# Kernel tuning notes

Hardware: AMD Instinct MI355X
Metric: run time of the kernel (lower is better)

## Reference

```python
import jax, jax.numpy as jnp
import numpy as np

N = 50000   # nodes
E = 800000  # edges
H = 128     # hidden dim
V = 50000   # feats_per_node (embedding vocab)


def setup_inputs() -> dict:
    key = jax.random.key(0)
    ks = jax.random.split(key, 16)
    s = 0.05  # keep activations in a sane range
    return {
        "node_ids": jax.random.randint(ks[0], (N,), 0, V),
        "src": jax.random.randint(ks[1], (E,), 0, N),
        "dst": jnp.sort(jax.random.randint(ks[2], (E,), 0, N)),
        "emb": jax.random.normal(ks[3], (V, H), jnp.float32) * s,
        "W_pool1": jax.random.normal(ks[4], (H, H), jnp.float32) * s,
        "b_pool1": jax.random.normal(ks[5], (H,), jnp.float32) * s,
        "W_self1": jax.random.normal(ks[6], (H, H), jnp.float32) * s,
        "W_neigh1": jax.random.normal(ks[7], (H, H), jnp.float32) * s,
        "b1": jax.random.normal(ks[8], (H,), jnp.float32) * s,
        "W_pool2": jax.random.normal(ks[9], (H, H), jnp.float32) * s,
        "b_pool2": jax.random.normal(ks[10], (H,), jnp.float32) * s,
        "W_self2": jax.random.normal(ks[11], (H, H), jnp.float32) * s,
        "W_neigh2": jax.random.normal(ks[12], (H, H), jnp.float32) * s,
        "b2": jax.random.normal(ks[13], (H,), jnp.float32) * s,
    }


def _sage_pool_layer(h, src, dst, W_pool, b_pool, W_self, W_neigh, b):
    # DGL SAGEConv('pool'): per-src MLP, gather over edges, segmented max per dst.
    m = jax.nn.relu(h @ W_pool + b_pool)              # [N, H]
    msgs = m[src]                                     # [E, H] gather
    agg = jax.ops.segment_max(msgs, dst, num_segments=N,
                              indices_are_sorted=True)  # [N, H]
    agg = jnp.where(jnp.isneginf(agg), 0.0, agg)      # zero-in-degree -> 0 (DGL semantics)
    return h @ W_self + agg @ W_neigh + b


def reference(node_ids, src, dst, emb,
              W_pool1, b_pool1, W_self1, W_neigh1, b1,
              W_pool2, b_pool2, W_self2, W_neigh2, b2):
    h = emb[node_ids]                                 # embedding_h on 1-hot indices
    h = _sage_pool_layer(h, src, dst, W_pool1, b_pool1, W_self1, W_neigh1, b1)
    h = _sage_pool_layer(h, src, dst, W_pool2, b_pool2, W_self2, W_neigh2, b2)
    return h
```

## Files before the change

### kernel.cpp

```cpp
#include <hip/hip_runtime.h>

#define HD 128

typedef __attribute__((ext_vector_type(8))) short short8;
typedef __attribute__((ext_vector_type(4))) float floatx4;

typedef unsigned short ushort_t;
typedef unsigned int uint_t;

__device__ __forceinline__ ushort_t f2b(float f) {
    union { float f; uint_t u; } v; v.f = f;
    uint_t r = v.u + 0x7fff + ((v.u >> 16) & 1);
    return (ushort_t)(r >> 16);
}
__device__ __forceinline__ float b_lo(uint_t p) {
    union { uint_t u; float f; } v; v.u = p << 16; return v.f;
}
__device__ __forceinline__ float b_hi(uint_t p) {
    union { uint_t u; float f; } v; v.u = p & 0xffff0000u; return v.f;
}
__device__ __forceinline__ uint_t packb(float a, float b) {
    union { float f; uint_t u; } x, y; x.f = a; y.f = b;
    return (x.u >> 16) | (y.u & 0xffff0000u);
}
__device__ __forceinline__ short8 cvt8(const float* __restrict__ p) {
    float4 u = *(const float4*)p, v = *(const float4*)(p + 4);
    short8 r;
    r[0] = (short)f2b(u.x); r[1] = (short)f2b(u.y); r[2] = (short)f2b(u.z); r[3] = (short)f2b(u.w);
    r[4] = (short)f2b(v.x); r[5] = (short)f2b(v.y); r[6] = (short)f2b(v.z); r[7] = (short)f2b(v.w);
    return r;
}

__global__ __launch_bounds__(256) void k_prep(const int* __restrict__ dst, int E,
                                              int* __restrict__ rp, int N,
                                              const float* W0, const float* W1,
                                              const float* W2, const float* W3,
                                              const float* W4, const float* W5,
                                              ushort_t* __restrict__ Wpk, int nbR) {
    int b = blockIdx.x;
    if (b < nbR) {
        int i = b * 256 + threadIdx.x;
        if (i > N) return;
        int lo = 0, hi = E;
        while (lo < hi) {
            int mid = (lo + hi) >> 1;
            if (dst[mid] < i) lo = mid + 1; else hi = mid;
        }
        rp[i] = lo;
    } else {
        int bb = b - nbR;
        const float* Ws[6] = {W0, W1, W2, W3, W4, W5};
        int mat = bb >> 6;
        int o = ((bb & 63) << 8) + threadIdx.x;
        int j = o & 7, l = (o >> 3) & 63, s = (o >> 9) & 3, t = o >> 11;
        int k = s * 32 + ((l >> 4) & 3) * 8 + j;
        int n = t * 16 + (l & 15);
        Wpk[(size_t)mat * 16384 + o] = f2b(Ws[mat][k * HD + n]);
    }
}

__device__ __forceinline__ void stage_w(const ushort_t* __restrict__ g,
                                        ushort_t* l, int tid) {
#pragma unroll
    for (int i = 0; i < 8; ++i) {
        int off = i * 2048 + tid * 8;
        *(short8*)&l[off] = *(const short8*)&g[off];
    }
}

__global__ __launch_bounds__(256) void k_gather_pool(const int* __restrict__ ids,
                                                     const float* __restrict__ emb,
                                                     const ushort_t* __restrict__ Wpk,
                                                     const float* __restrict__ bias,
                                                     ushort_t* __restrict__ h0,
                                                     ushort_t* __restrict__ m, int N) {
    __shared__ ushort_t Wl[16384];
    stage_w(Wpk, Wl, threadIdx.x);
    __syncthreads();

    int wave = blockIdx.x * 4 + (threadIdx.x >> 6);
    int row0 = wave * 32;
    if (row0 >= N) return;
    int l = threadIdx.x & 63;
    int ar0 = row0 + (l & 15); if (ar0 >= N) ar0 = N - 1;
    int ar1 = ar0 + 16;        if (ar1 >= N) ar1 = N - 1;
    int ac = (l >> 4) * 8;
    int id0 = ids[ar0], id1 = ids[ar1];
    short8 a0[4], a1[4];
#pragma unroll
    for (int s = 0; s < 4; ++s) {
        a0[s] = cvt8(&emb[(size_t)id0 * HD + s * 32 + ac]);
        a1[s] = cvt8(&emb[(size_t)id1 * HD + s * 32 + ac]);
        *(short8*)&h0[(size_t)ar0 * HD + s * 32 + ac] = a0[s];
        *(short8*)&h0[(size_t)ar1 * HD + s * 32 + ac] = a1[s];
    }
    int rb = row0 + (l >> 4) * 4;
#pragma unroll
    for (int t = 0; t < 8; ++t) {
        floatx4 acc0 = {0.f, 0.f, 0.f, 0.f};
        floatx4 acc1 = {0.f, 0.f, 0.f, 0.f};
#pragma unroll
        for (int s = 0; s < 4; ++s) {
            short8 b = *(const short8*)&Wl[(t * 4 + s) * 512 + l * 8];
            acc0 = __builtin_amdgcn_mfma_f32_16x16x32_bf16(a0[s], b, acc0, 0, 0, 0);
            acc1 = __builtin_amdgcn_mfma_f32_16x16x32_bf16(a1[s], b, acc1, 0, 0, 0);
        }
        int col = t * 16 + (l & 15);
        float bv = bias[col];
#pragma unroll
        for (int r = 0; r < 4; ++r) {
            int g0 = rb + r, g1 = rb + 16 + r;
            if (g0 < N) m[(size_t)g0 * HD + col] = f2b(fmaxf(acc0[r] + bv, 0.f));
            if (g1 < N) m[(size_t)g1 * HD + col] = f2b(fmaxf(acc1[r] + bv, 0.f));
        }
    }
}

__global__ __launch_bounds__(256) void k_pool(const ushort_t* __restrict__ h,
                                              const ushort_t* __restrict__ Wpk,
                                              const float* __restrict__ bias,
                                              ushort_t* __restrict__ m, int N) {
    __shared__ ushort_t Wl[16384];
    stage_w(Wpk, Wl, threadIdx.x);
    __syncthreads();

    int wave = blockIdx.x * 4 + (threadIdx.x >> 6);
    int row0 = wave * 32;
    if (row0 >= N) return;
    int l = threadIdx.x & 63;
    int ar0 = row0 + (l & 15); if (ar0 >= N) ar0 = N - 1;
    int ar1 = ar0 + 16;        if (ar1 >= N) ar1 = N - 1;
    int ac = (l >> 4) * 8;
    short8 a0[4], a1[4];
#pragma unroll
    for (int s = 0; s < 4; ++s) {
        a0[s] = *(const short8*)&h[(size_t)ar0 * HD + s * 32 + ac];
        a1[s] = *(const short8*)&h[(size_t)ar1 * HD + s * 32 + ac];
    }
    int rb = row0 + (l >> 4) * 4;
#pragma unroll
    for (int t = 0; t < 8; ++t) {
        floatx4 acc0 = {0.f, 0.f, 0.f, 0.f};
        floatx4 acc1 = {0.f, 0.f, 0.f, 0.f};
#pragma unroll
        for (int s = 0; s < 4; ++s) {
            short8 b = *(const short8*)&Wl[(t * 4 + s) * 512 + l * 8];
            acc0 = __builtin_amdgcn_mfma_f32_16x16x32_bf16(a0[s], b, acc0, 0, 0, 0);
            acc1 = __builtin_amdgcn_mfma_f32_16x16x32_bf16(a1[s], b, acc1, 0, 0, 0);
        }
        int col = t * 16 + (l & 15);
        float bv = bias[col];
#pragma unroll
        for (int r = 0; r < 4; ++r) {
            int g0 = rb + r, g1 = rb + 16 + r;
            if (g0 < N) m[(size_t)g0 * HD + col] = f2b(fmaxf(acc0[r] + bv, 0.f));
            if (g1 < N) m[(size_t)g1 * HD + col] = f2b(fmaxf(acc1[r] + bv, 0.f));
        }
    }
}

__global__ __launch_bounds__(256) void k_segmax(const ushort_t* __restrict__ m,
                                                const int* __restrict__ src,
                                                const int* __restrict__ rp,
                                                ushort_t* __restrict__ agg, int N) {
    int node = blockIdx.x * 4 + (threadIdx.x >> 6);
    if (node >= N) return;
    int l = threadIdx.x & 63;
    int half = l >> 5;
    int col4 = (l & 31) * 4;
    int beg = rp[node], end = rp[node + 1];
    float a0 = 0.f, a1 = 0.f, a2 = 0.f, a3 = 0.f;
    float c0 = 0.f, c1 = 0.f, c2 = 0.f, c3 = 0.f;
    int e = beg;
    for (; e + 8 <= end; e += 8) {
        int e0 = e + half, e1 = e + 2 + half, e2 = e + 4 + half, e3 = e + 6 + half;
        uint2 p0 = *(const uint2*)&m[(size_t)src[e0] * HD + col4];
        uint2 p1 = *(const uint2*)&m[(size_t)src[e1] * HD + col4];
        uint2 p2 = *(const uint2*)&m[(size_t)src[e2] * HD + col4];
        uint2 p3 = *(const uint2*)&m[(size_t)src[e3] * HD + col4];
        a0 = fmaxf(a0, b_lo(p0.x)); a1 = fmaxf(a1, b_hi(p0.x));
        a2 = fmaxf(a2, b_lo(p0.y)); a3 = fmaxf(a3, b_hi(p0.y));
        c0 = fmaxf(c0, b_lo(p1.x)); c1 = fmaxf(c1, b_hi(p1.x));
        c2 = fmaxf(c2, b_lo(p1.y)); c3 = fmaxf(c3, b_hi(p1.y));
        a0 = fmaxf(a0, b_lo(p2.x)); a1 = fmaxf(a1, b_hi(p2.x));
        a2 = fmaxf(a2, b_lo(p2.y)); a3 = fmaxf(a3, b_hi(p2.y));
        c0 = fmaxf(c0, b_lo(p3.x)); c1 = fmaxf(c1, b_hi(p3.x));
        c2 = fmaxf(c2, b_lo(p3.y)); c3 = fmaxf(c3, b_hi(p3.y));
    }
    for (; e < end; e += 2) {
        int ee = e + half; if (ee >= end) ee = end - 1;
        uint2 p = *(const uint2*)&m[(size_t)src[ee] * HD + col4];
        a0 = fmaxf(a0, b_lo(p.x)); a1 = fmaxf(a1, b_hi(p.x));
        a2 = fmaxf(a2, b_lo(p.y)); a3 = fmaxf(a3, b_hi(p.y));
    }
    a0 = fmaxf(a0, c0); a1 = fmaxf(a1, c1); a2 = fmaxf(a2, c2); a3 = fmaxf(a3, c3);
    a0 = fmaxf(a0, __shfl_xor(a0, 32));
    a1 = fmaxf(a1, __shfl_xor(a1, 32));
    a2 = fmaxf(a2, __shfl_xor(a2, 32));
    a3 = fmaxf(a3, __shfl_xor(a3, 32));
    if (half == 0) {
        uint2 o; o.x = packb(a0, a1); o.y = packb(a2, a3);
        *(uint2*)&agg[(size_t)node * HD + col4] = o;
    }
}

template <bool F32OUT>
__global__ __launch_bounds__(256) void k_dual(const ushort_t* __restrict__ h,
                                              const ushort_t* __restrict__ agg,
                                              const ushort_t* __restrict__ WsPk,
                                              const ushort_t* __restrict__ WnPk,
                                              const float* __restrict__ bias,
                                              void* __restrict__ outp, int N) {
    __shared__ ushort_t Wl[32768];
    stage_w(WsPk, Wl, threadIdx.x);
    stage_w(WnPk, Wl + 16384, threadIdx.x);
    __syncthreads();

    int wave = blockIdx.x * 4 + (threadIdx.x >> 6);
    int row0 = wave * 32;
    if (row0 >= N) return;
    int l = threadIdx.x & 63;
    int ar0 = row0 + (l & 15); if (ar0 >= N) ar0 = N - 1;
    int ar1 = ar0 + 16;        if (ar1 >= N) ar1 = N - 1;
    int ac = (l >> 4) * 8;
    short8 ah0[4], ah1[4], ag0[4], ag1[4];
#pragma unroll
    for (int s = 0; s < 4; ++s) {
        ah0[s] = *(const short8*)&h[(size_t)ar0 * HD + s * 32 + ac];
        ah1[s] = *(const short8*)&h[(size_t)ar1 * HD + s * 32 + ac];
        ag0[s] = *(const short8*)&agg[(size_t)ar0 * HD + s * 32 + ac];
        ag1[s] = *(const short8*)&agg[(size_t)ar1 * HD + s * 32 + ac];
    }
    int rb = row0 + (l >> 4) * 4;
#pragma unroll
    for (int t = 0; t < 8; ++t) {
        floatx4 acc0 = {0.f, 0.f, 0.f, 0.f};
        floatx4 acc1 = {0.f, 0.f, 0.f, 0.f};
#pragma unroll
        for (int s = 0; s < 4; ++s) {
            short8 bs = *(const short8*)&Wl[(t * 4 + s) * 512 + l * 8];
            acc0 = __builtin_amdgcn_mfma_f32_16x16x32_bf16(ah0[s], bs, acc0, 0, 0, 0);
            acc1 = __builtin_amdgcn_mfma_f32_16x16x32_bf16(ah1[s], bs, acc1, 0, 0, 0);
        }
#pragma unroll
        for (int s = 0; s < 4; ++s) {
            short8 bn = *(const short8*)&Wl[16384 + (t * 4 + s) * 512 + l * 8];
            acc0 = __builtin_amdgcn_mfma_f32_16x16x32_bf16(ag0[s], bn, acc0, 0, 0, 0);
            acc1 = __builtin_amdgcn_mfma_f32_16x16x32_bf16(ag1[s], bn, acc1, 0, 0, 0);
        }
        int col = t * 16 + (l & 15);
        float bv = bias[col];
#pragma unroll
        for (int r = 0; r < 4; ++r) {
            int g0 = rb + r, g1 = rb + 16 + r;
            float v0 = acc0[r] + bv, v1 = acc1[r] + bv;
            if (F32OUT) {
                if (g0 < N) ((float*)outp)[(size_t)g0 * HD + col] = v0;
                if (g1 < N) ((float*)outp)[(size_t)g1 * HD + col] = v1;
            } else {
                if (g0 < N) ((ushort_t*)outp)[(size_t)g0 * HD + col] = f2b(v0);
                if (g1 < N) ((ushort_t*)outp)[(size_t)g1 * HD + col] = f2b(v1);
            }
        }
    }
}

extern "C" void kernel_launch(void* const* d_in, const int* in_sizes, int n_in,
                              void* d_out, int out_size, void* d_ws, size_t ws_size,
                              hipStream_t stream) {
    const int*   node_ids = (const int*)d_in[0];
    const int*   src      = (const int*)d_in[1];
    const int*   dst      = (const int*)d_in[2];
    const float* emb      = (const float*)d_in[3];
    const float* Wp1      = (const float*)d_in[4];
    const float* bp1      = (const float*)d_in[5];
    const float* Ws1      = (const float*)d_in[6];
    const float* Wn1      = (const float*)d_in[7];
    const float* b1       = (const float*)d_in[8];
    const float* Wp2      = (const float*)d_in[9];
    const float* bp2      = (const float*)d_in[10];
    const float* Ws2      = (const float*)d_in[11];
    const float* Wn2      = (const float*)d_in[12];
    const float* b2       = (const float*)d_in[13];
    float* out = (float*)d_out;

    const int N = in_sizes[0];
    const int E = in_sizes[1];

    char* ws = (char*)d_ws;
    int* rp = (int*)ws;
    size_t off = (((size_t)(N + 1) * 4) + 255) & ~(size_t)255;
    ushort_t* Wpk  = (ushort_t*)(ws + off);
    ushort_t* h0   = Wpk + 6 * 16384;
    ushort_t* h1   = h0 + (size_t)N * HD;
    ushort_t* bufM = h1 + (size_t)N * HD;
    ushort_t* bufA = bufM + (size_t)N * HD;

    const int nbR = (N + 1 + 255) / 256;
    const int nbP = 6 * 64;
    const int nb_gemm = (N + 127) / 128;
    const int nb_seg  = (N + 3) / 4;

    k_prep<<<nbR + nbP, 256, 0, stream>>>(dst, E, rp, N,
                                          Wp1, Ws1, Wn1, Wp2, Ws2, Wn2, Wpk, nbR);

    const ushort_t* Wp1k = Wpk;
    const ushort_t* Ws1k = Wpk + 16384;
    const ushort_t* Wn1k = Wpk + 2 * 16384;
    const ushort_t* Wp2k = Wpk + 3 * 16384;
    const ushort_t* Ws2k = Wpk + 4 * 16384;
    const ushort_t* Wn2k = Wpk + 5 * 16384;

    k_gather_pool<<<nb_gemm, 256, 0, stream>>>(node_ids, emb, Wp1k, bp1, h0, bufM, N);
    k_segmax<<<nb_seg, 256, 0, stream>>>(bufM, src, rp, bufA, N);
    k_dual<false><<<nb_gemm, 256, 0, stream>>>(h0, bufA, Ws1k, Wn1k, b1, h1, N);
    k_pool<<<nb_gemm, 256, 0, stream>>>(h1, Wp2k, bp2, bufM, N);
    k_segmax<<<nb_seg, 256, 0, stream>>>(bufM, src, rp, bufA, N);
    k_dual<true><<<nb_gemm, 256, 0, stream>>>(h1, bufA, Ws2k, Wn2k, b2, out, N);
}
```

Baseline: 236.7 us.

## Transpose MFMA operands for vectorized row stores; widen segmax gathers to 16B

The GEMM kernels swap the MFMA A/B operands so each lane holds four consecutive output columns of one row. The epilogue can then write packed 8-byte bf16 or 16-byte fp32 vectors with a float4 bias load, replacing scattered 2-byte and 4-byte stores. The segmented-max kernel now gathers 16 bytes per lane, with four edges in flight per wave instead of two. That needs an extra shuffle stage and more registers, and wastes more lanes on low-degree tails.

```diff
diff --git a/kernel.cpp b/kernel.cpp
--- a/kernel.cpp
+++ b/kernel.cpp
@@ -68,6 +68,17 @@
     }
 }
 
+__device__ __forceinline__ void store_bf16(ushort_t* __restrict__ m, int row,
+                                           int colbase, const floatx4& acc,
+                                           const float4& bv, bool relu, int N) {
+    if (row >= N) return;
+    float v0 = acc[0] + bv.x, v1 = acc[1] + bv.y, v2 = acc[2] + bv.z, v3 = acc[3] + bv.w;
+    if (relu) { v0 = fmaxf(v0, 0.f); v1 = fmaxf(v1, 0.f); v2 = fmaxf(v2, 0.f); v3 = fmaxf(v3, 0.f); }
+    uint2 o; o.x = (uint_t)f2b(v0) | ((uint_t)f2b(v1) << 16);
+    o.y = (uint_t)f2b(v2) | ((uint_t)f2b(v3) << 16);
+    *(uint2*)&m[(size_t)row * HD + colbase] = o;
+}
+
 __global__ __launch_bounds__(256) void k_gather_pool(const int* __restrict__ ids,
                                                      const float* __restrict__ emb,
                                                      const ushort_t* __restrict__ Wpk,
@@ -94,25 +105,22 @@
         *(short8*)&h0[(size_t)ar0 * HD + s * 32 + ac] = a0[s];
         *(short8*)&h0[(size_t)ar1 * HD + s * 32 + ac] = a1[s];
     }
-    int rb = row0 + (l >> 4) * 4;
+    int g0 = row0 + (l & 15), g1 = g0 + 16;
+    int cb0 = ((l >> 4) & 3) * 4;
 #pragma unroll
     for (int t = 0; t < 8; ++t) {
         floatx4 acc0 = {0.f, 0.f, 0.f, 0.f};
         floatx4 acc1 = {0.f, 0.f, 0.f, 0.f};
 #pragma unroll
         for (int s = 0; s < 4; ++s) {
-            short8 b = *(const short8*)&Wl[(t * 4 + s) * 512 + l * 8];
-            acc0 = __builtin_amdgcn_mfma_f32_16x16x32_bf16(a0[s], b, acc0, 0, 0, 0);
-            acc1 = __builtin_amdgcn_mfma_f32_16x16x32_bf16(a1[s], b, acc1, 0, 0, 0);
-        }
-        int col = t * 16 + (l & 15);
-        float bv = bias[col];
-#pragma unroll
-        for (int r = 0; r < 4; ++r) {
-            int g0 = rb + r, g1 = rb + 16 + r;
-            if (g0 < N) m[(size_t)g0 * HD + col] = f2b(fmaxf(acc0[r] + bv, 0.f));
-            if (g1 < N) m[(size_t)g1 * HD + col] = f2b(fmaxf(acc1[r] + bv, 0.f));
-        }
+            short8 w = *(const short8*)&Wl[(t * 4 + s) * 512 + l * 8];
+            acc0 = __builtin_amdgcn_mfma_f32_16x16x32_bf16(w, a0[s], acc0, 0, 0, 0);
+            acc1 = __builtin_amdgcn_mfma_f32_16x16x32_bf16(w, a1[s], acc1, 0, 0, 0);
+        }
+        int cb = t * 16 + cb0;
+        float4 bv = *(const float4*)&bias[cb];
+        store_bf16(m, g0, cb, acc0, bv, true, N);
+        store_bf16(m, g1, cb, acc1, bv, true, N);
     }
 }
 
@@ -137,25 +145,22 @@
         a0[s] = *(const short8*)&h[(size_t)ar0 * HD + s * 32 + ac];
         a1[s] = *(const short8*)&h[(size_t)ar1 * HD + s * 32 + ac];
     }
-    int rb = row0 + (l >> 4) * 4;
+    int g0 = row0 + (l & 15), g1 = g0 + 16;
+    int cb0 = ((l >> 4) & 3) * 4;
 #pragma unroll
     for (int t = 0; t < 8; ++t) {
         floatx4 acc0 = {0.f, 0.f, 0.f, 0.f};
         floatx4 acc1 = {0.f, 0.f, 0.f, 0.f};
 #pragma unroll
         for (int s = 0; s < 4; ++s) {
-            short8 b = *(const short8*)&Wl[(t * 4 + s) * 512 + l * 8];
-            acc0 = __builtin_amdgcn_mfma_f32_16x16x32_bf16(a0[s], b, acc0, 0, 0, 0);
-            acc1 = __builtin_amdgcn_mfma_f32_16x16x32_bf16(a1[s], b, acc1, 0, 0, 0);
-        }
-        int col = t * 16 + (l & 15);
-        float bv = bias[col];
-#pragma unroll
-        for (int r = 0; r < 4; ++r) {
-            int g0 = rb + r, g1 = rb + 16 + r;
-            if (g0 < N) m[(size_t)g0 * HD + col] = f2b(fmaxf(acc0[r] + bv, 0.f));
-            if (g1 < N) m[(size_t)g1 * HD + col] = f2b(fmaxf(acc1[r] + bv, 0.f));
-        }
+            short8 w = *(const short8*)&Wl[(t * 4 + s) * 512 + l * 8];
+            acc0 = __builtin_amdgcn_mfma_f32_16x16x32_bf16(w, a0[s], acc0, 0, 0, 0);
+            acc1 = __builtin_amdgcn_mfma_f32_16x16x32_bf16(w, a1[s], acc1, 0, 0, 0);
+        }
+        int cb = t * 16 + cb0;
+        float4 bv = *(const float4*)&bias[cb];
+        store_bf16(m, g0, cb, acc0, bv, true, N);
+        store_bf16(m, g1, cb, acc1, bv, true, N);
     }
 }
 
@@ -166,41 +171,53 @@
     int node = blockIdx.x * 4 + (threadIdx.x >> 6);
     if (node >= N) return;
     int l = threadIdx.x & 63;
-    int half = l >> 5;
-    int col4 = (l & 31) * 4;
+    int slot = l >> 4;
+    int col8 = (l & 15) * 8;
     int beg = rp[node], end = rp[node + 1];
-    float a0 = 0.f, a1 = 0.f, a2 = 0.f, a3 = 0.f;
-    float c0 = 0.f, c1 = 0.f, c2 = 0.f, c3 = 0.f;
+    float a[8] = {0.f, 0.f, 0.f, 0.f, 0.f, 0.f, 0.f, 0.f};
+    float c[8] = {0.f, 0.f, 0.f, 0.f, 0.f, 0.f, 0.f, 0.f};
     int e = beg;
-    for (; e + 8 <= end; e += 8) {
-        int e0 = e + half, e1 = e + 2 + half, e2 = e + 4 + half, e3 = e + 6 + half;
-        uint2 p0 = *(const uint2*)&m[(size_t)src[e0] * HD + col4];
-        uint2 p1 = *(const uint2*)&m[(size_t)src[e1] * HD + col4];
-        uint2 p2 = *(const uint2*)&m[(size_t)src[e2] * HD + col4];
-        uint2 p3 = *(const uint2*)&m[(size_t)src[e3] * HD + col4];
-        a0 = fmaxf(a0, b_lo(p0.x)); a1 = fmaxf(a1, b_hi(p0.x));
-        a2 = fmaxf(a2, b_lo(p0.y)); a3 = fmaxf(a3, b_hi(p0.y));
-        c0 = fmaxf(c0, b_lo(p1.x)); c1 = fmaxf(c1, b_hi(p1.x));
-        c2 = fmaxf(c2, b_lo(p1.y)); c3 = fmaxf(c3, b_hi(p1.y));
-        a0 = fmaxf(a0, b_lo(p2.x)); a1 = fmaxf(a1, b_hi(p2.x));
-        a2 = fmaxf(a2, b_lo(p2.y)); a3 = fmaxf(a3, b_hi(p2.y));
-        c0 = fmaxf(c0, b_lo(p3.x)); c1 = fmaxf(c1, b_hi(p3.x));
-        c2 = fmaxf(c2, b_lo(p3.y)); c3 = fmaxf(c3, b_hi(p3.y));
-    }
-    for (; e < end; e += 2) {
-        int ee = e + half; if (ee >= end) ee = end - 1;
-        uint2 p = *(const uint2*)&m[(size_t)src[ee] * HD + col4];
-        a0 = fmaxf(a0, b_lo(p.x)); a1 = fmaxf(a1, b_hi(p.x));
-        a2 = fmaxf(a2, b_lo(p.y)); a3 = fmaxf(a3, b_hi(p.y));
-    }
-    a0 = fmaxf(a0, c0); a1 = fmaxf(a1, c1); a2 = fmaxf(a2, c2); a3 = fmaxf(a3, c3);
-    a0 = fmaxf(a0, __shfl_xor(a0, 32));
-    a1 = fmaxf(a1, __shfl_xor(a1, 32));
-    a2 = fmaxf(a2, __shfl_xor(a2, 32));
-    a3 = fmaxf(a3, __shfl_xor(a3, 32));
-    if (half == 0) {
-        uint2 o; o.x = packb(a0, a1); o.y = packb(a2, a3);
-        *(uint2*)&agg[(size_t)node * HD + col4] = o;
+    for (; e + 16 <= end; e += 16) {
+        uint4 p0 = *(const uint4*)&m[(size_t)src[e + slot] * HD + col8];
+        uint4 p1 = *(const uint4*)&m[(size_t)src[e + 4 + slot] * HD + col8];
+        uint4 p2 = *(const uint4*)&m[(size_t)src[e + 8 + slot] * HD + col8];
+        uint4 p3 = *(const uint4*)&m[(size_t)src[e + 12 + slot] * HD + col8];
+        a[0] = fmaxf(a[0], b_lo(p0.x)); a[1] = fmaxf(a[1], b_hi(p0.x));
+        a[2] = fmaxf(a[2], b_lo(p0.y)); a[3] = fmaxf(a[3], b_hi(p0.y));
+        a[4] = fmaxf(a[4], b_lo(p0.z)); a[5] = fmaxf(a[5], b_hi(p0.z));
+        a[6] = fmaxf(a[6], b_lo(p0.w)); a[7] = fmaxf(a[7], b_hi(p0.w));
+        c[0] = fmaxf(c[0], b_lo(p1.x)); c[1] = fmaxf(c[1], b_hi(p1.x));
+        c[2] = fmaxf(c[2], b_lo(p1.y)); c[3] = fmaxf(c[3], b_hi(p1.y));
+        c[4] = fmaxf(c[4], b_lo(p1.z)); c[5] = fmaxf(c[5], b_hi(p1.z));
+        c[6] = fmaxf(c[6], b_lo(p1.w)); c[7] = fmaxf(c[7], b_hi(p1.w));
+        a[0] = fmaxf(a[0], b_lo(p2.x)); a[1] = fmaxf(a[1], b_hi(p2.x));
+        a[2] = fmaxf(a[2], b_lo(p2.y)); a[3] = fmaxf(a[3], b_hi(p2.y));
+        a[4] = fmaxf(a[4], b_lo(p2.z)); a[5] = fmaxf(a[5], b_hi(p2.z));
+        a[6] = fmaxf(a[6], b_lo(p2.w)); a[7] = fmaxf(a[7], b_hi(p2.w));
+        c[0] = fmaxf(c[0], b_lo(p3.x)); c[1] = fmaxf(c[1], b_hi(p3.x));
+        c[2] = fmaxf(c[2], b_lo(p3.y)); c[3] = fmaxf(c[3], b_hi(p3.y));
+        c[4] = fmaxf(c[4], b_lo(p3.z)); c[5] = fmaxf(c[5], b_hi(p3.z));
+        c[6] = fmaxf(c[6], b_lo(p3.w)); c[7] = fmaxf(c[7], b_hi(p3.w));
+    }
+    for (; e < end; e += 4) {
+        int ee = e + slot; if (ee >= end) ee = end - 1;
+        uint4 p = *(const uint4*)&m[(size_t)src[ee] * HD + col8];
+        a[0] = fmaxf(a[0], b_lo(p.x)); a[1] = fmaxf(a[1], b_hi(p.x));
+        a[2] = fmaxf(a[2], b_lo(p.y)); a[3] = fmaxf(a[3], b_hi(p.y));
+        a[4] = fmaxf(a[4], b_lo(p.z)); a[5] = fmaxf(a[5], b_hi(p.z));
+        a[6] = fmaxf(a[6], b_lo(p.w)); a[7] = fmaxf(a[7], b_hi(p.w));
+    }
+#pragma unroll
+    for (int i = 0; i < 8; ++i) {
+        a[i] = fmaxf(a[i], c[i]);
+        a[i] = fmaxf(a[i], __shfl_xor(a[i], 16));
+        a[i] = fmaxf(a[i], __shfl_xor(a[i], 32));
+    }
+    if (slot == 0) {
+        uint4 o;
+        o.x = packb(a[0], a[1]); o.y = packb(a[2], a[3]);
+        o.z = packb(a[4], a[5]); o.w = packb(a[6], a[7]);
+        *(uint4*)&agg[(size_t)node * HD + col8] = o;
     }
 }
 
@@ -231,36 +248,42 @@
         ag0[s] = *(const short8*)&agg[(size_t)ar0 * HD + s * 32 + ac];
         ag1[s] = *(const short8*)&agg[(size_t)ar1 * HD + s * 32 + ac];
     }
-    int rb = row0 + (l >> 4) * 4;
+    int g0 = row0 + (l & 15), g1 = g0 + 16;
+    int cb0 = ((l >> 4) & 3) * 4;
 #pragma unroll
     for (int t = 0; t < 8; ++t) {
         floatx4 acc0 = {0.f, 0.f, 0.f, 0.f};
         floatx4 acc1 = {0.f, 0.f, 0.f, 0.f};
 #pragma unroll
         for (int s = 0; s < 4; ++s) {
-            short8 bs = *(const short8*)&Wl[(t * 4 + s) * 512 + l * 8];
-            acc0 = __builtin_amdgcn_mfma_f32_16x16x32_bf16(ah0[s], bs, acc0, 0, 0, 0);
-            acc1 = __builtin_amdgcn_mfma_f32_16x16x32_bf16(ah1[s], bs, acc1, 0, 0, 0);
+            short8 ws = *(const short8*)&Wl[(t * 4 + s) * 512 + l * 8];
+            acc0 = __builtin_amdgcn_mfma_f32_16x16x32_bf16(ws, ah0[s], acc0, 0, 0, 0);
+            acc1 = __builtin_amdgcn_mfma_f32_16x16x32_bf16(ws, ah1[s], acc1, 0, 0, 0);
         }
 #pragma unroll
         for (int s = 0; s < 4; ++s) {
-            short8 bn = *(const short8*)&Wl[16384 + (t * 4 + s) * 512 + l * 8];
-            acc0 = __builtin_amdgcn_mfma_f32_16x16x32_bf16(ag0[s], bn, acc0, 0, 0, 0);
-            acc1 = __builtin_amdgcn_mfma_f32_16x16x32_bf16(ag1[s], bn, acc1, 0, 0, 0);
-        }
-        int col = t * 16 + (l & 15);
-        float bv = bias[col];
-#pragma unroll
-        for (int r = 0; r < 4; ++r) {
-            int g0 = rb + r, g1 = rb + 16 + r;
-            float v0 = acc0[r] + bv, v1 = acc1[r] + bv;
-            if (F32OUT) {
-                if (g0 < N) ((float*)outp)[(size_t)g0 * HD + col] = v0;
-                if (g1 < N) ((float*)outp)[(size_t)g1 * HD + col] = v1;
-            } else {
-                if (g0 < N) ((ushort_t*)outp)[(size_t)g0 * HD + col] = f2b(v0);
-                if (g1 < N) ((ushort_t*)outp)[(size_t)g1 * HD + col] = f2b(v1);
+            short8 wn = *(const short8*)&Wl[16384 + (t * 4 + s) * 512 + l * 8];
+            acc0 = __builtin_amdgcn_mfma_f32_16x16x32_bf16(wn, ag0[s], acc0, 0, 0, 0);
+            acc1 = __builtin_amdgcn_mfma_f32_16x16x32_bf16(wn, ag1[s], acc1, 0, 0, 0);
+        }
+        int cb = t * 16 + cb0;
+        float4 bv = *(const float4*)&bias[cb];
+        if (F32OUT) {
+            float* out = (float*)outp;
+            if (g0 < N) {
+                float4 v = make_float4(acc0[0] + bv.x, acc0[1] + bv.y,
+                                       acc0[2] + bv.z, acc0[3] + bv.w);
+                *(float4*)&out[(size_t)g0 * HD + cb] = v;
             }
+            if (g1 < N) {
+                float4 v = make_float4(acc1[0] + bv.x, acc1[1] + bv.y,
+                                       acc1[2] + bv.z, acc1[3] + bv.w);
+                *(float4*)&out[(size_t)g1 * HD + cb] = v;
+            }
+        } else {
+            ushort_t* out = (ushort_t*)outp;
+            store_bf16(out, g0, cb, acc0, bv, false, N);
+            store_bf16(out, g1, cb, acc1, bv, false, N);
         }
     }
 }
```

After: 222.7 us. -5.9%, faster.
